# Performance work log

Hardware: AMD Instinct MI355X
Metric: run time of the kernel (lower is better)

Reference implementation:

```python
import jax, jax.numpy as jnp
import numpy as np

D_MODEL = 2048
N_HEADS = 16
GKV = 4
D_FF = 8192
D_HEAD = D_MODEL // N_HEADS
EPS = 1e-6


def rmsnorm(x, w):
    ms = jnp.mean(x * x, axis=-1, keepdims=True)
    return x * jax.lax.rsqrt(ms + EPS) * w


def attention(q, k, v, mask=None):
    # q: (B,Tq,H,d), k/v: (B,Tk,H,d)
    scale = 1.0 / jnp.sqrt(jnp.asarray(q.shape[-1], q.dtype))
    scores = jnp.einsum('bqhd,bkhd->bhqk', q, k) * scale
    if mask is not None:
        scores = scores + mask
    probs = jax.nn.softmax(scores, axis=-1)
    return jnp.einsum('bhqk,bkhd->bqhd', probs, v)


def setup_inputs() -> dict:
    key = jax.random.key(0)
    ks = jax.random.split(key, 12)
    B, T = 2, 2048
    s = 0.02
    return {
        'x': jax.random.normal(ks[0], (B, T, D_MODEL), jnp.float32),
        'k_ctx': jax.random.normal(ks[1], (B, T, GKV, D_HEAD), jnp.float32),
        'v_ctx': jax.random.normal(ks[2], (B, T, GKV, D_HEAD), jnp.float32),
        # cross-attn params (weights stored as (in, out); y = x @ W)
        'wq': jax.random.normal(ks[3], (D_MODEL, D_MODEL), jnp.float32) * s,
        'wo_cross': jax.random.normal(ks[4], (D_MODEL, D_MODEL), jnp.float32) * s,
        'norm_q_w': jnp.ones((D_MODEL,), jnp.float32),
        # self-attn params
        'wqkv': jax.random.normal(ks[5], (D_MODEL, 3 * D_MODEL), jnp.float32) * s,
        'wo_self': jax.random.normal(ks[6], (D_MODEL, D_MODEL), jnp.float32) * s,
        'norm_qkv_w': jnp.ones((D_MODEL,), jnp.float32),
        # FFN params (bias=False in FeedForward)
        'ffn_w1': jax.random.normal(ks[7], (D_MODEL, D_FF), jnp.float32) * s,
        'ffn_w2': jax.random.normal(ks[8], (D_FF, D_MODEL), jnp.float32) * s,
        'ffn_norm_w': jnp.ones((D_MODEL,), jnp.float32),
    }


def reference(x, k_ctx, v_ctx, wq, wo_cross, norm_q_w, wqkv, wo_self,
              norm_qkv_w, ffn_w1, ffn_w2, ffn_norm_w):
    B, T, D = x.shape
    repeat = N_HEADS // GKV

    # ---- cross attention (GQA) ----
    q = (rmsnorm(x, norm_q_w) @ wq).reshape(B, T, N_HEADS, D_HEAD)
    k = jnp.repeat(k_ctx, repeat, axis=2)  # (B,Tk,H,d), matches repeat_interleave
    v = jnp.repeat(v_ctx, repeat, axis=2)
    ctx = attention(q, k, v, mask=None).reshape(B, T, D)
    x = x + ctx @ wo_cross

    # ---- causal self attention ----
    xn = rmsnorm(x, norm_qkv_w)
    qkv = xn @ wqkv
    qs, ks_, vs = jnp.split(qkv, 3, axis=-1)
    qs = qs.reshape(B, T, N_HEADS, D_HEAD)
    ks_ = ks_.reshape(B, T, N_HEADS, D_HEAD)
    vs = vs.reshape(B, T, N_HEADS, D_HEAD)
    causal_mask = jnp.triu(jnp.full((T, T), -jnp.inf, x.dtype), k=1)[None, None]
    ctx2 = attention(qs, ks_, vs, mask=causal_mask).reshape(B, T, D)
    x = x + ctx2 @ wo_self

    # ---- FFN (SiLU) ----
    h = rmsnorm(x, ffn_norm_w)
    y = jax.nn.silu(h @ ffn_w1) @ ffn_w2
    return x + y
```

## Files before the change

kernel.cpp:

```cpp
#include <hip/hip_runtime.h>
#include <math.h>

typedef unsigned short u16;
typedef __attribute__((ext_vector_type(4))) u16 u16x4;
typedef __attribute__((ext_vector_type(8))) u16 u16x8;
typedef __attribute__((ext_vector_type(8))) __bf16 bf16x8;
typedef __attribute__((ext_vector_type(4))) float f32x4;
typedef __attribute__((ext_vector_type(16))) float f32x16;
typedef __attribute__((ext_vector_type(4))) unsigned u32x4;

#define D_MODEL 2048
#define SEQ 2048
#define BATCH 2
#define NH 16
#define HD 128
#define DFF 8192
#define ROWS (BATCH * SEQ)

__device__ __forceinline__ u16 f2bf(float f) {
  union { float f; unsigned u; } v; v.f = f;
  unsigned r = v.u + 0x7FFFu + ((v.u >> 16) & 1u);
  return (u16)(r >> 16);
}
__device__ __forceinline__ u16 to_bf16(float f) { return f2bf(f); }
__device__ __forceinline__ u16 to_bf16(u16 v) { return v; }

__device__ __forceinline__ f32x4 mfma16(u16x8 a, u16x8 b, f32x4 c) {
  return __builtin_amdgcn_mfma_f32_16x16x32_bf16(
      __builtin_bit_cast(bf16x8, a), __builtin_bit_cast(bf16x8, b), c, 0, 0, 0);
}
__device__ __forceinline__ f32x16 mfma32(u16x8 a, u16x8 b, f32x16 c) {
  return __builtin_amdgcn_mfma_f32_32x32x16_bf16(
      __builtin_bit_cast(bf16x8, a), __builtin_bit_cast(bf16x8, b), c, 0, 0, 0);
}

__device__ __forceinline__ void gll16(const void* g, void* l) {
  __builtin_amdgcn_global_load_lds(
      (const __attribute__((address_space(1))) void*)g,
      (__attribute__((address_space(3))) void*)l, 16, 0, 0);
}

__global__ __launch_bounds__(256) void cast_kernel(const float* __restrict__ in,
                                                   u16* __restrict__ out, int n8) {
  int i = blockIdx.x * 256 + threadIdx.x;
  if (i >= n8) return;
  const float4* p = (const float4*)in + (size_t)i * 2;
  float4 a = p[0], b = p[1];
  u16x8 o;
  o[0] = f2bf(a.x); o[1] = f2bf(a.y); o[2] = f2bf(a.z); o[3] = f2bf(a.w);
  o[4] = f2bf(b.x); o[5] = f2bf(b.y); o[6] = f2bf(b.z); o[7] = f2bf(b.w);
  *((u16x8*)out + i) = o;
}

struct WTArgs {
  const float* src[6];
  u16* dst[6];
  int K[6], N[6];
  int start[7];
};

__global__ __launch_bounds__(256) void cast_transpose_all(WTArgs a) {
  __shared__ float tile[64][69];
  int b = blockIdx.x;
  int wi = 0;
#pragma unroll
  for (int i = 0; i < 6; ++i)
    if (b >= a.start[i + 1]) wi = i + 1;
  const float* src = a.src[wi];
  u16* dst = a.dst[wi];
  int K = a.K[wi], N = a.N[wi];
  int t = b - a.start[wi];
  int cols = N >> 6;
  int n0 = (t % cols) * 64, k0 = (t / cols) * 64;
  int rr = threadIdx.x >> 4, cc = (threadIdx.x & 15) * 4;
#pragma unroll
  for (int pp = 0; pp < 4; ++pp) {
    int kk = pp * 16 + rr;
    *(float4*)&tile[kk][cc] = *(const float4*)(src + (size_t)(k0 + kk) * N + n0 + cc);
  }
  __syncthreads();
#pragma unroll
  for (int pp = 0; pp < 4; ++pp) {
    int d = pp * 16 + rr;
    u16x4 w;
#pragma unroll
    for (int j = 0; j < 4; ++j) w[j] = f2bf(tile[cc + j][d]);
    *(u16x4*)(dst + (size_t)(n0 + d) * K + k0 + cc) = w;
  }
}

template <typename ST>
__global__ __launch_bounds__(256) void build_vt_kernel(
    const ST* __restrict__ src, u16* __restrict__ dst, int HZ,
    size_t src_b_stride, size_t src_h_stride, int src_tok_stride) {
  __shared__ u16 tl[64][72];
  int z = blockIdx.z, zb = z / HZ, zh = z % HZ;
  const ST* s = src + (size_t)zb * src_b_stride + (size_t)zh * src_h_stride;
  int t0 = blockIdx.x * 64, d0 = blockIdx.y * 64;
  int rr = threadIdx.x >> 4, cc = (threadIdx.x & 15) * 4;
#pragma unroll
  for (int pp = 0; pp < 4; ++pp) {
    int t = pp * 16 + rr;
    const ST* sp = s + (size_t)(t0 + t) * src_tok_stride + d0 + cc;
#pragma unroll
    for (int j = 0; j < 4; ++j) tl[t][cc + j] = to_bf16(sp[j]);
  }
  __syncthreads();
  u16* dp = dst + (size_t)z * HD * SEQ;
#pragma unroll
  for (int pp = 0; pp < 4; ++pp) {
    int d = pp * 16 + rr;
    u16x4 w;
#pragma unroll
    for (int j = 0; j < 4; ++j) w[j] = tl[cc + j][d];
    *(u16x4*)(dp + (size_t)(d0 + d) * SEQ + t0 + cc) = w;
  }
}

__global__ __launch_bounds__(256) void rmsnorm_kernel(const float* __restrict__ x,
                                                      const float* __restrict__ w,
                                                      u16* __restrict__ out) {
  __shared__ float red[4];
  int row = blockIdx.x, t = threadIdx.x;
  const float4* xr = (const float4*)(x + (size_t)row * D_MODEL);
  float4 a = xr[t * 2], b = xr[t * 2 + 1];
  float ss = a.x * a.x + a.y * a.y + a.z * a.z + a.w * a.w +
             b.x * b.x + b.y * b.y + b.z * b.z + b.w * b.w;
#pragma unroll
  for (int m = 1; m < 64; m <<= 1) ss += __shfl_xor(ss, m, 64);
  if ((t & 63) == 0) red[t >> 6] = ss;
  __syncthreads();
  float tot = red[0] + red[1] + red[2] + red[3];
  float sc = rsqrtf(tot * (1.0f / D_MODEL) + 1e-6f);
  const float4* wr = (const float4*)w;
  float4 wa = wr[t * 2], wb = wr[t * 2 + 1];
  u16x8 o;
  o[0] = f2bf(a.x * sc * wa.x); o[1] = f2bf(a.y * sc * wa.y);
  o[2] = f2bf(a.z * sc * wa.z); o[3] = f2bf(a.w * sc * wa.w);
  o[4] = f2bf(b.x * sc * wb.x); o[5] = f2bf(b.y * sc * wb.y);
  o[6] = f2bf(b.z * sc * wb.z); o[7] = f2bf(b.w * sc * wb.w);
  *((u16x8*)(out + (size_t)row * D_MODEL) + t) = o;
}

template <int MODE>
__global__ __launch_bounds__(256) void combine_kernel(
    const float* __restrict__ p0, const float* __restrict__ p1,
    const float* __restrict__ res, void* __restrict__ outv, int n4) {
  int i = blockIdx.x * 256 + threadIdx.x;
  if (i >= n4) return;
  float4 a = ((const float4*)p0)[i];
  float4 b = ((const float4*)p1)[i];
  if (MODE == 1) {
    float4 r = ((const float4*)res)[i];
    float4 o;
    o.x = r.x + a.x + b.x; o.y = r.y + a.y + b.y;
    o.z = r.z + a.z + b.z; o.w = r.w + a.w + b.w;
    ((float4*)outv)[i] = o;
  } else {
    u16x4 o;
    o[0] = f2bf(a.x + b.x); o[1] = f2bf(a.y + b.y);
    o[2] = f2bf(a.z + b.z); o[3] = f2bf(a.w + b.w);
    ((u16x4*)outv)[i] = o;
  }
}

#define LOADFRAGS(BASE)                                                        \
  {                                                                            \
    const u16* SA = S + (BASE);                                                \
    const u16* SB = SA + 8192;                                                 \
    _Pragma("unroll") for (int m = 0; m < 8; ++m) {                            \
      int row = wm * 128 + m * 16 + r16;                                       \
      aF[m] = *(const u16x8*)(SA + row * 32 + ((kg ^ ((row >> 1) & 3)) << 3)); \
    }                                                                          \
    _Pragma("unroll") for (int n = 0; n < 4; ++n) {                            \
      int row = wn * 64 + n * 16 + r16;                                        \
      bF[n] = *(const u16x8*)(SB + row * 32 + ((kg ^ ((row >> 1) & 3)) << 3)); \
    }                                                                          \
  }

#define MFMA_HALF(HH)                                                          \
  __builtin_amdgcn_s_setprio(1);                                               \
  _Pragma("unroll") for (int m = 0; m < 8; ++m) {                              \
    acc[m][2 * (HH)] = mfma16(aF[m], bF[2 * (HH)], acc[m][2 * (HH)]);          \
    acc[m][2 * (HH) + 1] =                                                     \
        mfma16(aF[m], bF[2 * (HH) + 1], acc[m][2 * (HH) + 1]);                 \
  }                                                                            \
  __builtin_amdgcn_s_setprio(0);

#define GPH_E(T, P, VM, ISSUE, FIRST)                                          \
  {                                                                            \
    if (ISSUE) issue_half(4 * (T) + (P) + 4);                                  \
    asm volatile("s_waitcnt vmcnt(" #VM ")" ::: "memory");                     \
    __builtin_amdgcn_sched_barrier(0);                                         \
    __builtin_amdgcn_s_barrier();                                              \
    if (FIRST) LOADFRAGS((((((T) & 1) << 2) | (P)) << 13));                    \
    MFMA_HALF(0)                                                               \
    __builtin_amdgcn_s_barrier();                                              \
  }

#define GPH_O(T, P, VM, ISSUE, PF)                                             \
  {                                                                            \
    if (ISSUE) issue_half(4 * (T) + (P) + 4);                                  \
    asm volatile("s_waitcnt vmcnt(" #VM ")" ::: "memory");                     \
    __builtin_amdgcn_sched_barrier(0);                                         \
    __builtin_amdgcn_s_barrier();                                              \
    MFMA_HALF(1)                                                               \
    if (PF) {                                                                  \
      if ((P) == 1) {                                                          \
        LOADFRAGS((((((T) & 1) << 2) | 2) << 13));                             \
      } else {                                                                 \
        LOADFRAGS(((((T) + 1) & 1) << 2) << 13);                               \
      }                                                                        \
    }                                                                          \
    __builtin_amdgcn_s_barrier();                                              \
  }

template <int EPI, int SPLIT>
__global__ __launch_bounds__(512, 1) void gemm256_kernel(
    const u16* __restrict__ A, const u16* __restrict__ Bt, void* __restrict__ Cv,
    float* __restrict__ Cv2, const float* __restrict__ res, int N, int K) {
  __shared__ __align__(16) u16 S[8 * 8192];
  const int tid = threadIdx.x, lane = tid & 63, wave = tid >> 6;
  const int wm = wave >> 2, wn = wave & 3;
  const int r16 = lane & 15, kg = lane >> 4;
  const int cols = N >> 8;
  const int cpx = gridDim.x >> 3;
  const int bid = blockIdx.x;
  const int swz = (bid & 7) * cpx + (bid >> 3);
  const int tiles = gridDim.x / SPLIT;
  const int tile = swz % tiles, kslice = swz / tiles;
  const int bm = (tile / cols) * 256, bn = (tile % cols) * 256;
  const int Ksub = K / SPLIT;
  const int koff = kslice * Ksub;
  const int nt = Ksub >> 6;

  auto issue_half = [&](int h) {
    int p = h & 3, t = h >> 2;
    const u16* src = (p & 1) ? (Bt + (size_t)bn * K) : (A + (size_t)bm * K);
    int kbase = koff + t * 64 + (p >> 1) * 32;
    u16* ldst = S + ((((t & 1) << 2) | p) << 13);
#pragma unroll
    for (int i = 0; i < 2; ++i) {
      int c = i * 512 + tid;
      int row = c >> 2, ch = c & 3;
      int kc = ch ^ ((row >> 1) & 3);
      gll16(src + (size_t)row * K + kbase + kc * 8, ldst + c * 8);
    }
  };

  u16x8 aF[8], bF[4];
  f32x4 acc[8][4] = {};

  issue_half(0); issue_half(1); issue_half(2); issue_half(3);
  GPH_E(0, 0, 6, true, true);
  GPH_O(0, 1, 4, true, true);
  GPH_E(0, 2, 6, true, false);
  GPH_O(0, 3, 4, true, true);
  for (int t = 1; t < nt - 1; ++t) {
    GPH_E(t, 0, 6, true, false);
    GPH_O(t, 1, 4, true, true);
    GPH_E(t, 2, 6, true, false);
    GPH_O(t, 3, 4, true, true);
  }
  {
    const int t = nt - 1;
    GPH_E(t, 0, 6, false, false);
    GPH_O(t, 1, 0, false, true);
    GPH_E(t, 2, 0, false, false);
    GPH_O(t, 3, 0, false, false);
  }

  float* Pp = (EPI == 3) ? (kslice ? Cv2 : (float*)Cv) : nullptr;
#pragma unroll
  for (int m = 0; m < 8; ++m) {
    int r0 = bm + wm * 128 + m * 16 + kg * 4;
#pragma unroll
    for (int n = 0; n < 4; ++n) {
      int cc = bn + wn * 64 + n * 16 + r16;
#pragma unroll
      for (int r = 0; r < 4; ++r) {
        size_t idx = (size_t)(r0 + r) * N + cc;
        float v = acc[m][n][r];
        if (EPI == 3) {
          Pp[idx] = v;
        } else if (EPI == 1) {
          ((float*)Cv)[idx] = res[idx] + v;
        } else if (EPI == 0) {
          ((u16*)Cv)[idx] = f2bf(v);
        } else {
          float s = v / (1.0f + __expf(-v));
          ((u16*)Cv)[idx] = f2bf(s);
        }
      }
    }
  }
}

#define NPH2(T, P, VM, ISSUE)                                                  \
  {                                                                            \
    if (ISSUE) issue_pair(2 * (T) + (P) + 1);                                  \
    asm volatile("s_waitcnt vmcnt(" #VM ")" ::: "memory");                     \
    __builtin_amdgcn_sched_barrier(0);                                         \
    __builtin_amdgcn_s_barrier();                                              \
    const u16* SA = S + (((2 * (T) + (P)) & 1) * 12288);                       \
    const u16* SB = SA + 8192;                                                 \
    u16x8 aF[4], bF[4];                                                        \
    _Pragma("unroll") for (int m = 0; m < 4; ++m) {                            \
      int row = wm * 64 + m * 16 + r16;                                        \
      aF[m] = *(const u16x8*)(SA + row * 32 + ((kg ^ ((row >> 1) & 3)) << 3)); \
    }                                                                          \
    _Pragma("unroll") for (int n = 0; n < 4; ++n) {                            \
      int row = wn * 64 + n * 16 + r16;                                        \
      bF[n] = *(const u16x8*)(SB + row * 32 + ((kg ^ ((row >> 1) & 3)) << 3)); \
    }                                                                          \
    __builtin_amdgcn_s_setprio(1);                                             \
    _Pragma("unroll") for (int m = 0; m < 4; ++m)                              \
      _Pragma("unroll") for (int n = 0; n < 4; ++n)                            \
        acc[m][n] = mfma16(aF[m], bF[n], acc[m][n]);                           \
    __builtin_amdgcn_s_setprio(0);                                             \
    __builtin_amdgcn_s_barrier();                                              \
  }

template <int EPI>
__global__ __launch_bounds__(512, 4) void gemm_n128_kernel(
    const u16* __restrict__ A, const u16* __restrict__ Bt, void* __restrict__ Cv,
    const float* __restrict__ res, u16* __restrict__ vt, int N, int K) {
  __shared__ __align__(16) u16 S[2 * 12288];
  const int tid = threadIdx.x, lane = tid & 63, wave = tid >> 6;
  const int wm = wave >> 1, wn = wave & 1;
  const int r16 = lane & 15, kg = lane >> 4;
  const int cols = N >> 7;
  const int cpx = gridDim.x >> 3;
  const int bid = blockIdx.x;
  const int swz = (bid & 7) * cpx + (bid >> 3);
  const int bm = (swz / cols) * 256, bn = (swz % cols) * 128;
  const int nt = K >> 6;

  auto issue_pair = [&](int g) {
    int p = g & 1, t = g >> 1;
    int kbase = t * 64 + p * 32;
    u16* reg = S + ((g & 1) * 12288);
#pragma unroll
    for (int i = 0; i < 2; ++i) {
      int c = i * 512 + tid;
      int row = c >> 2, ch = c & 3;
      int kc = ch ^ ((row >> 1) & 3);
      gll16(A + (size_t)(bm + row) * K + kbase + kc * 8, reg + c * 8);
    }
    {
      int row = tid >> 2, ch = tid & 3;
      int kc = ch ^ ((row >> 1) & 3);
      gll16(Bt + (size_t)(bn + row) * K + kbase + kc * 8, reg + 8192 + tid * 8);
    }
  };

  f32x4 acc[4][4] = {};

  issue_pair(0);
  for (int t = 0; t < nt - 1; ++t) {
    NPH2(t, 0, 3, true);
    NPH2(t, 1, 3, true);
  }
  NPH2(nt - 1, 0, 3, true);
  NPH2(nt - 1, 1, 0, false);

  const bool vmode = (EPI == 4) && (bn >= 4096);
#pragma unroll
  for (int m = 0; m < 4; ++m) {
    int r0 = bm + wm * 64 + m * 16 + kg * 4;
#pragma unroll
    for (int n = 0; n < 4; ++n) {
      int cc = bn + wn * 64 + n * 16 + r16;
      if (vmode) {
        int c2 = cc - 4096;
        int z = (r0 >> 11) * NH + (c2 >> 7);
        int d = c2 & 127;
        int t0 = r0 & (SEQ - 1);
        u16x4 w;
#pragma unroll
        for (int r = 0; r < 4; ++r) w[r] = f2bf(acc[m][n][r]);
        *(u16x4*)(vt + ((size_t)z * HD + d) * SEQ + t0) = w;
      } else {
#pragma unroll
        for (int r = 0; r < 4; ++r) {
          size_t idx = (size_t)(r0 + r) * N + cc;
          float v = acc[m][n][r];
          if (EPI == 1) {
            ((float*)Cv)[idx] = res[idx] + v;
          } else {
            ((u16*)Cv)[idx] = f2bf(v);
          }
        }
      }
    }
  }
}

template <bool CAUSAL, bool SELF>
__global__ __launch_bounds__(512, 2) void attn2_kernel(
    const u16* __restrict__ qp, const u16* __restrict__ kp,
    const u16* __restrict__ vtp, u16* __restrict__ outp) {
  __shared__ __align__(16) u16 Kl[2 * 64 * 128];
  __shared__ __align__(16) u16 Vl[2 * 128 * 64];
  const int tid = threadIdx.x, lane = tid & 63, wave = tid >> 6;
  const int lo = lane & 31, hi = lane >> 5;
  const int qt = blockIdx.x, bh = blockIdx.y, b = bh >> 4, h = bh & 15;
  const int qw0 = qt * 256 + wave * 32;
  const int qg = qw0 + lo;
  const size_t qstr = SELF ? 6144 : 2048;
  const size_t kstr = SELF ? 6144 : 512;
  const u16* qbase = qp + ((size_t)b * SEQ + qg) * qstr + h * HD;
  const u16* kbase = kp + (size_t)b * SEQ * kstr + (SELF ? (2048 + h * HD) : ((h >> 2) * HD));
  const u16* vbase = vtp + (size_t)(SELF ? (b * NH + h) : (b * 4 + (h >> 2))) * HD * SEQ;

  u16x8 qf[8];
#pragma unroll
  for (int dc = 0; dc < 8; ++dc) qf[dc] = *(const u16x8*)(qbase + dc * 16 + hi * 8);

  f32x16 o[4] = {};
  float m_run = -3e38f, l_run = 0.f;
  const int ntiles = CAUSAL ? qt * 4 + 4 : SEQ / 64;
  const float scale = 0.088388347648318447f;
  const float defer_thr = 90.50966799187809f;

  auto stage = [&](int kt, int buf) {
#pragma unroll
    for (int i = 0; i < 2; ++i) {
      int c = i * 512 + tid;
      int krow = c >> 4, ks = c & 15;
      gll16(kbase + (size_t)(kt * 64 + krow) * kstr + ((ks ^ (krow & 15)) * 8),
            Kl + (size_t)buf * 8192 + (size_t)c * 8);
      int vd = c >> 3, vs = c & 7;
      gll16(vbase + (size_t)vd * SEQ + kt * 64 + ((vs ^ (vd & 7)) * 8),
            Vl + (size_t)buf * 8192 + (size_t)c * 8);
    }
  };

  stage(0, 0);
  stage(1, 1);

  for (int kt = 0; kt < ntiles; ++kt) {
    if (kt + 1 < ntiles) {
      asm volatile("s_waitcnt vmcnt(4)" ::: "memory");
    } else {
      asm volatile("s_waitcnt vmcnt(0)" ::: "memory");
    }
    __builtin_amdgcn_sched_barrier(0);
    __syncthreads();
    const u16* Kb = Kl + (size_t)(kt & 1) * 8192;
    const u16* Vb = Vl + (size_t)(kt & 1) * 8192;

    if (!(CAUSAL && kt * 64 > qw0 + 31)) {
      f32x16 s01[2] = {};
#pragma unroll
      for (int k2 = 0; k2 < 2; ++k2) {
        int key = k2 * 32 + lo;
#pragma unroll
        for (int mf = 0; mf < 8; ++mf) {
          int dc = mf * 2 + hi;
          u16x8 kf = *(const u16x8*)(Kb + key * 128 + ((dc ^ (key & 15)) * 8));
          s01[k2] = mfma32(kf, qf[mf], s01[k2]);
        }
      }

      float sv[32];
      float pm = -3e38f;
#pragma unroll
      for (int k2 = 0; k2 < 2; ++k2)
#pragma unroll
        for (int r = 0; r < 16; ++r) {
          float v = s01[k2][r];
          if (CAUSAL) {
            int key = kt * 64 + k2 * 32 + (r & 3) + 8 * (r >> 2) + 4 * hi;
            if (key > qg) v = -3e38f;
          }
          sv[k2 * 16 + r] = v;
          pm = fmaxf(pm, v);
        }
      pm = fmaxf(pm, __shfl_xor(pm, 32, 64));

      const bool defer = __all(pm - m_run <= defer_thr);
      float mn = defer ? m_run : fmaxf(m_run, pm);
      float corr = defer ? 1.0f : __expf((m_run - mn) * scale);
      m_run = mn;

      float ps = 0.f;
      u16x8 pf[4];
#pragma unroll
      for (int k2 = 0; k2 < 2; ++k2)
#pragma unroll
        for (int hf = 0; hf < 2; ++hf) {
          float p8[8];
#pragma unroll
          for (int j = 0; j < 8; ++j) {
            p8[j] = __expf((sv[k2 * 16 + hf * 8 + j] - mn) * scale);
            ps += p8[j];
          }
          unsigned w0, w1, w2, w3;
          asm("v_cvt_pk_bf16_f32 %0, %1, %2" : "=v"(w0) : "v"(p8[0]), "v"(p8[1]));
          asm("v_cvt_pk_bf16_f32 %0, %1, %2" : "=v"(w1) : "v"(p8[2]), "v"(p8[3]));
          asm("v_cvt_pk_bf16_f32 %0, %1, %2" : "=v"(w2) : "v"(p8[4]), "v"(p8[5]));
          asm("v_cvt_pk_bf16_f32 %0, %1, %2" : "=v"(w3) : "v"(p8[6]), "v"(p8[7]));
          asm("v_permlane32_swap_b32 %0, %1" : "+v"(w0), "+v"(w2));
          asm("v_permlane32_swap_b32 %0, %1" : "+v"(w1), "+v"(w3));
          u32x4 fr; fr[0] = w0; fr[1] = w1; fr[2] = w2; fr[3] = w3;
          pf[k2 * 2 + hf] = __builtin_bit_cast(u16x8, fr);
        }
      ps += __shfl_xor(ps, 32, 64);

      if (defer) {
        l_run += ps;
      } else {
        l_run = l_run * corr + ps;
#pragma unroll
        for (int mb = 0; mb < 4; ++mb)
#pragma unroll
          for (int r = 0; r < 16; ++r) o[mb][r] *= corr;
      }

#pragma unroll
      for (int kc = 0; kc < 4; ++kc) {
        int vcs = kc * 2 + hi;
#pragma unroll
        for (int mb = 0; mb < 4; ++mb) {
          int d = mb * 32 + lo;
          u16x8 vf = *(const u16x8*)(Vb + d * 64 + ((vcs ^ (d & 7)) * 8));
          o[mb] = mfma32(vf, pf[kc], o[mb]);
        }
      }
    }

    __syncthreads();
    if (kt + 2 < ntiles) stage(kt + 2, kt & 1);
  }

  float inv = 1.0f / l_run;
  u16* ob = outp + ((size_t)b * SEQ + qg) * D_MODEL + h * HD + 4 * hi;
#pragma unroll
  for (int mb = 0; mb < 4; ++mb)
#pragma unroll
    for (int rq = 0; rq < 4; ++rq) {
      u16x4 w;
#pragma unroll
      for (int j = 0; j < 4; ++j) w[j] = f2bf(o[mb][rq * 4 + j] * inv);
      *(u16x4*)(ob + mb * 32 + rq * 8) = w;
    }
}

extern "C" void kernel_launch(void* const* d_in, const int* in_sizes, int n_in,
                              void* d_out, int out_size, void* d_ws, size_t ws_size,
                              hipStream_t stream) {
  const float* x          = (const float*)d_in[0];
  const float* k_ctx      = (const float*)d_in[1];
  const float* v_ctx      = (const float*)d_in[2];
  const float* wq         = (const float*)d_in[3];
  const float* wo_cross   = (const float*)d_in[4];
  const float* norm_q_w   = (const float*)d_in[5];
  const float* wqkv       = (const float*)d_in[6];
  const float* wo_self    = (const float*)d_in[7];
  const float* norm_qkv_w = (const float*)d_in[8];
  const float* ffn_w1     = (const float*)d_in[9];
  const float* ffn_w2     = (const float*)d_in[10];
  const float* ffn_norm_w = (const float*)d_in[11];
  float* out = (float*)d_out;

  char* ws = (char*)d_ws;
  size_t off = 0;
  auto alloc_u16 = [&](size_t n) { u16* p = (u16*)(ws + off); off += n * 2; return p; };
  auto alloc_f32 = [&](size_t n) { float* p = (float*)(ws + off); off += n * 4; return p; };
  u16* wq_bf   = alloc_u16((size_t)2048 * 2048);
  u16* woc_bf  = alloc_u16((size_t)2048 * 2048);
  u16* wqkv_bf = alloc_u16((size_t)2048 * 6144);
  u16* wos_bf  = alloc_u16((size_t)2048 * 2048);
  u16* w1_bf   = alloc_u16((size_t)2048 * 8192);
  u16* w2_bf   = alloc_u16((size_t)8192 * 2048);
  u16* xn_bf   = alloc_u16((size_t)ROWS * 2048);
  u16* qkv_bf  = alloc_u16((size_t)ROWS * 6144);
  u16* attn_bf = alloc_u16((size_t)ROWS * 2048);
  float* x1    = alloc_f32((size_t)ROWS * 2048);
  float* x2    = alloc_f32((size_t)ROWS * 2048);
  u16* q_bf    = qkv_bf;
  u16* h1_bf   = qkv_bf;
  u16* kc_bf   = (u16*)x2;
  u16* vt_ctx  = kc_bf + (size_t)BATCH * SEQ * 4 * HD;
  u16* vt_self = (u16*)x2;
  const int n4 = ROWS * 2048 / 4;

  {
    WTArgs wt;
    const float* s6[6] = {wq, wo_cross, wqkv, wo_self, ffn_w1, ffn_w2};
    u16* d6[6] = {wq_bf, woc_bf, wqkv_bf, wos_bf, w1_bf, w2_bf};
    int K6[6] = {2048, 2048, 2048, 2048, 2048, 8192};
    int N6[6] = {2048, 2048, 6144, 2048, 8192, 2048};
    int s = 0;
    wt.start[0] = 0;
    for (int i = 0; i < 6; ++i) {
      wt.src[i] = s6[i]; wt.dst[i] = d6[i]; wt.K[i] = K6[i]; wt.N[i] = N6[i];
      s += (N6[i] >> 6) * (K6[i] >> 6);
      wt.start[i + 1] = s;
    }
    cast_transpose_all<<<dim3(s), 256, 0, stream>>>(wt);
  }
  {
    int n8 = (int)((size_t)BATCH * SEQ * 4 * HD / 8);
    cast_kernel<<<dim3((n8 + 255) / 256), dim3(256), 0, stream>>>(k_ctx, kc_bf, n8);
  }
  build_vt_kernel<float><<<dim3(SEQ / 64, HD / 64, BATCH * 4), 256, 0, stream>>>(
      v_ctx, vt_ctx, 4, (size_t)SEQ * 512, (size_t)HD, 512);

  rmsnorm_kernel<<<ROWS, 256, 0, stream>>>(x, norm_q_w, xn_bf);
  gemm_n128_kernel<0><<<dim3((ROWS / 256) * (2048 / 128)), 512, 0, stream>>>(
      xn_bf, wq_bf, q_bf, nullptr, nullptr, 2048, 2048);
  attn2_kernel<false, false><<<dim3(SEQ / 256, BATCH * NH), 512, 0, stream>>>(
      q_bf, kc_bf, vt_ctx, attn_bf);
  gemm_n128_kernel<1><<<dim3((ROWS / 256) * (2048 / 128)), 512, 0, stream>>>(
      attn_bf, woc_bf, x1, x, nullptr, 2048, 2048);

  rmsnorm_kernel<<<ROWS, 256, 0, stream>>>(x1, norm_qkv_w, xn_bf);
  gemm_n128_kernel<4><<<dim3((ROWS / 256) * (6144 / 128)), 512, 0, stream>>>(
      xn_bf, wqkv_bf, qkv_bf, nullptr, vt_self, 6144, 2048);
  attn2_kernel<true, true><<<dim3(SEQ / 256, BATCH * NH), 512, 0, stream>>>(
      qkv_bf, qkv_bf, vt_self, attn_bf);
  gemm_n128_kernel<1><<<dim3((ROWS / 256) * (2048 / 128)), 512, 0, stream>>>(
      attn_bf, wos_bf, x2, x1, nullptr, 2048, 2048);

  rmsnorm_kernel<<<ROWS, 256, 0, stream>>>(x2, ffn_norm_w, xn_bf);
  gemm256_kernel<2, 1><<<dim3((ROWS / 256) * (8192 / 256)), 512, 0, stream>>>(
      xn_bf, w1_bf, h1_bf, nullptr, nullptr, 8192, 2048);
  gemm256_kernel<3, 2><<<dim3(256), 512, 0, stream>>>(
      h1_bf, w2_bf, out, x1, nullptr, 2048, 8192);
  combine_kernel<1><<<dim3((n4 + 255) / 256), 256, 0, stream>>>(
      out, x1, x2, out, n4);
}
```

Before: 814.8 us.

## Double-buffer GEMM register fragments to overlap LDS reads with MFMA

The 256x256 GEMM main loop now keeps two register sets of A/B fragments. The next k-half's fragments are loaded from LDS into the alternate set while MFMAs run on the current set, and the vmcnt waits in even phases are dropped. The aim is to hide LDS read latency behind matrix math. It roughly doubles the fragment register footprint and leans on the remaining barriers and waitcnts to keep the LDS data ordered correctly.

```diff
diff --git a/kernel.cpp b/kernel.cpp
--- a/kernel.cpp
+++ b/kernel.cpp
@@ -164,54 +164,45 @@
   }
 }
 
-#define LOADFRAGS(BASE)                                                        \
+#define LOADSET(AF, BF, BASE)                                                  \
   {                                                                            \
     const u16* SA = S + (BASE);                                                \
     const u16* SB = SA + 8192;                                                 \
     _Pragma("unroll") for (int m = 0; m < 8; ++m) {                            \
       int row = wm * 128 + m * 16 + r16;                                       \
-      aF[m] = *(const u16x8*)(SA + row * 32 + ((kg ^ ((row >> 1) & 3)) << 3)); \
+      AF[m] = *(const u16x8*)(SA + row * 32 + ((kg ^ ((row >> 1) & 3)) << 3)); \
     }                                                                          \
     _Pragma("unroll") for (int n = 0; n < 4; ++n) {                            \
       int row = wn * 64 + n * 16 + r16;                                        \
-      bF[n] = *(const u16x8*)(SB + row * 32 + ((kg ^ ((row >> 1) & 3)) << 3)); \
+      BF[n] = *(const u16x8*)(SB + row * 32 + ((kg ^ ((row >> 1) & 3)) << 3)); \
     }                                                                          \
   }
 
-#define MFMA_HALF(HH)                                                          \
+#define MHALF(AF, BF, HH)                                                      \
   __builtin_amdgcn_s_setprio(1);                                               \
   _Pragma("unroll") for (int m = 0; m < 8; ++m) {                              \
-    acc[m][2 * (HH)] = mfma16(aF[m], bF[2 * (HH)], acc[m][2 * (HH)]);          \
+    acc[m][2 * (HH)] = mfma16(AF[m], BF[2 * (HH)], acc[m][2 * (HH)]);          \
     acc[m][2 * (HH) + 1] =                                                     \
-        mfma16(aF[m], bF[2 * (HH) + 1], acc[m][2 * (HH) + 1]);                 \
+        mfma16(AF[m], BF[2 * (HH) + 1], acc[m][2 * (HH) + 1]);                 \
   }                                                                            \
   __builtin_amdgcn_s_setprio(0);
 
-#define GPH_E(T, P, VM, ISSUE, FIRST)                                          \
+#define PH_EVEN(T, P, ISSUE, AF, BF)                                           \
+  {                                                                            \
+    if (ISSUE) issue_half(4 * (T) + (P) + 4);                                  \
+    __builtin_amdgcn_s_barrier();                                              \
+    MHALF(AF, BF, 0)                                                           \
+    __builtin_amdgcn_s_barrier();                                              \
+  }
+
+#define PH_ODD(T, P, VM, ISSUE, DOLOAD, AF, BF, LAF, LBF, LBASE)               \
   {                                                                            \
     if (ISSUE) issue_half(4 * (T) + (P) + 4);                                  \
     asm volatile("s_waitcnt vmcnt(" #VM ")" ::: "memory");                     \
     __builtin_amdgcn_sched_barrier(0);                                         \
     __builtin_amdgcn_s_barrier();                                              \
-    if (FIRST) LOADFRAGS((((((T) & 1) << 2) | (P)) << 13));                    \
-    MFMA_HALF(0)                                                               \
-    __builtin_amdgcn_s_barrier();                                              \
-  }
-
-#define GPH_O(T, P, VM, ISSUE, PF)                                             \
-  {                                                                            \
-    if (ISSUE) issue_half(4 * (T) + (P) + 4);                                  \
-    asm volatile("s_waitcnt vmcnt(" #VM ")" ::: "memory");                     \
-    __builtin_amdgcn_sched_barrier(0);                                         \
-    __builtin_amdgcn_s_barrier();                                              \
-    MFMA_HALF(1)                                                               \
-    if (PF) {                                                                  \
-      if ((P) == 1) {                                                          \
-        LOADFRAGS((((((T) & 1) << 2) | 2) << 13));                             \
-      } else {                                                                 \
-        LOADFRAGS(((((T) + 1) & 1) << 2) << 13);                               \
-      }                                                                        \
-    }                                                                          \
+    if (DOLOAD) LOADSET(LAF, LBF, LBASE);                                      \
+    MHALF(AF, BF, 1)                                                           \
     __builtin_amdgcn_s_barrier();                                              \
   }
 
@@ -248,26 +239,31 @@
     }
   };
 
-  u16x8 aF[8], bF[4];
+  u16x8 aF0[8], bF0[4], aF1[8], bF1[4];
   f32x4 acc[8][4] = {};
 
   issue_half(0); issue_half(1); issue_half(2); issue_half(3);
-  GPH_E(0, 0, 6, true, true);
-  GPH_O(0, 1, 4, true, true);
-  GPH_E(0, 2, 6, true, false);
-  GPH_O(0, 3, 4, true, true);
-  for (int t = 1; t < nt - 1; ++t) {
-    GPH_E(t, 0, 6, true, false);
-    GPH_O(t, 1, 4, true, true);
-    GPH_E(t, 2, 6, true, false);
-    GPH_O(t, 3, 4, true, true);
+  asm volatile("s_waitcnt vmcnt(4)" ::: "memory");
+  __builtin_amdgcn_sched_barrier(0);
+  __builtin_amdgcn_s_barrier();
+  LOADSET(aF0, bF0, 0);
+
+  for (int t = 0; t < nt - 1; ++t) {
+    PH_EVEN(t, 0, true, aF0, bF0);
+    PH_ODD(t, 1, 4, true, true, aF0, bF0, aF1, bF1, ((((t) & 1) << 2) | 2) << 13);
+    PH_EVEN(t, 2, true, aF1, bF1);
+    PH_ODD(t, 3, 4, true, true, aF1, bF1, aF0, bF0, ((((t) + 1) & 1) << 2) << 13);
   }
   {
     const int t = nt - 1;
-    GPH_E(t, 0, 6, false, false);
-    GPH_O(t, 1, 0, false, true);
-    GPH_E(t, 2, 0, false, false);
-    GPH_O(t, 3, 0, false, false);
+    PH_EVEN(t, 0, false, aF0, bF0);
+    PH_ODD(t, 1, 0, false, true, aF0, bF0, aF1, bF1, ((((t) & 1) << 2) | 2) << 13);
+    PH_EVEN(t, 2, false, aF1, bF1);
+    {
+      __builtin_amdgcn_s_barrier();
+      MHALF(aF1, bF1, 1)
+      __builtin_amdgcn_s_barrier();
+    }
   }
 
   float* Pp = (EPI == 3) ? (kslice ? Cv2 : (float*)Cv) : nullptr;
```

Measured after the change: 816.7 us. Within noise of the previous version (+0.2%).
